# Kernel tuning notes

Measured on AMD Instinct MI355X. Metric: run time of the kernel, lower is better.

Reference implementation:

```python
import jax, jax.numpy as jnp
import numpy as np

HEADS = 20
NUM_AOE = 16
NUM_IP = 16


def setup_inputs() -> dict:
    key = jax.random.key(0)
    ks = jax.random.split(key, 7)
    B, Sq, H = 8, 4096, 1280
    Skv, C = 109, 768
    scale = 0.02
    return {
        "hidden_states": jax.random.normal(ks[0], (B, Sq, H), jnp.float32),
        "encoder_hidden_states": jax.random.normal(ks[1], (B, Skv, C), jnp.float32),
        "Wq": jax.random.normal(ks[2], (H, H), jnp.float32) * scale,
        "Wk": jax.random.normal(ks[3], (C, H), jnp.float32) * scale,
        "Wv": jax.random.normal(ks[4], (C, H), jnp.float32) * scale,
        "Wo": jax.random.normal(ks[5], (H, H), jnp.float32) * scale,
        "bo": jnp.zeros((H,), jnp.float32),
    }


def reference(hidden_states, encoder_hidden_states, Wq, Wk, Wv, Wo, bo):
    B, Sq, H = hidden_states.shape
    Skv = encoder_hidden_states.shape[1]
    head_dim = H // HEADS
    residual = hidden_states

    # projections (no bias on q/k/v, as in diffusers SD attention)
    q = (hidden_states @ Wq).reshape(B, Sq, HEADS, head_dim).transpose(0, 2, 1, 3)
    k = (encoder_hidden_states @ Wk).reshape(B, Skv, HEADS, head_dim).transpose(0, 2, 1, 3)
    v = (encoder_hidden_states @ Wv).reshape(B, Skv, HEADS, head_dim).transpose(0, 2, 1, 3)

    # manual attention: QK^T / sqrt(d), softmax
    scores = jnp.einsum("bhqd,bhkd->bhqk", q, k) / jnp.sqrt(jnp.asarray(head_dim, q.dtype))
    probs = jax.nn.softmax(scores, axis=-1)

    # frequency_mode != 'both': rescale aoe (first NUM_AOE) and image (last NUM_IP)
    # key-token ranges post-softmax, then renormalize. scale_aoe = scale_ip = 1
    # in this config, but the renormalization math is kept faithfully.
    scale_aoe = jnp.asarray(1.0, probs.dtype)
    scale_ip = jnp.asarray(1.0, probs.dtype)
    idx = jnp.arange(Skv)
    scale_vector = jnp.where(idx < NUM_AOE, scale_aoe, 1.0)
    scale_vector = jnp.where(idx >= Skv - NUM_IP, scale_vector * scale_ip, scale_vector)
    probs = probs * scale_vector  # broadcasts over (B, HEADS, Sq, Skv)
    probs = probs / probs.sum(axis=-1, keepdims=True)

    out = jnp.einsum("bhqk,bhkd->bhqd", probs, v)
    out = out.transpose(0, 2, 1, 3).reshape(B, Sq, H)
    out = out @ Wo + bo
    # residual connection, rescale_output_factor = 1.0
    return out + residual
```

## Files before the change

### kernel.cpp

```cpp
#include <hip/hip_runtime.h>
#include <hip/hip_bf16.h>

typedef unsigned short u16;
typedef __attribute__((ext_vector_type(8))) short short8;
typedef __attribute__((ext_vector_type(4))) short short4v;
typedef __attribute__((ext_vector_type(4))) float f32x4;

#define HEADS 20
#define HD 64
#define BB 8
#define SQ 4096
#define HDIM 1280
#define SKV 109
#define CDIM 768
#define SKV_PAD 128
#define SKV_T 112

#define SBAR() asm volatile("s_barrier" ::: "memory")

static __device__ __forceinline__ u16 f2bf(float x) {
  union { __hip_bfloat16 h; u16 u; } cv;
  cv.h = __float2bfloat16(x);
  return cv.u;
}

static __device__ __forceinline__ void gll16(const void* g, void* l) {
  __builtin_amdgcn_global_load_lds(
      (const __attribute__((address_space(1))) unsigned int*)g,
      (__attribute__((address_space(3))) unsigned int*)l, 16, 0, 0);
}

__global__ __launch_bounds__(256) void tcvt(const float* __restrict__ W,
                                            u16* __restrict__ out, int K, int N,
                                            float scale) {
  __shared__ float t[32][33];
  int tx = threadIdx.x & 31, ty = threadIdx.x >> 5;
  int n0 = blockIdx.x * 32, k0 = blockIdx.y * 32;
#pragma unroll
  for (int i = 0; i < 32; i += 8)
    t[ty + i][tx] = W[(size_t)(k0 + ty + i) * N + n0 + tx];
  __syncthreads();
#pragma unroll
  for (int i = 0; i < 32; i += 8)
    out[(size_t)(n0 + ty + i) * K + k0 + tx] = f2bf(t[tx][ty + i] * scale);
}

__global__ __launch_bounds__(256) void ehs_prep(const float* __restrict__ e,
                                                u16* __restrict__ out) {
  int idx = blockIdx.x * 256 + threadIdx.x;
  if (idx >= BB * SKV_PAD * CDIM / 4) return;
  int c4 = idx * 4;
  int b = c4 / (SKV_PAD * CDIM);
  int rem = c4 - b * (SKV_PAD * CDIM);
  int s = rem / CDIM;
  int c = rem - s * CDIM;
  short4v o = {0, 0, 0, 0};
  if (s < SKV) {
    f32x4 v = *(const f32x4*)(e + ((size_t)b * SKV + s) * CDIM + c);
#pragma unroll
    for (int j = 0; j < 4; j++) o[j] = (short)f2bf(v[j]);
  }
  *(short4v*)&out[c4] = o;
}

__global__ __launch_bounds__(256) void hscvt(const float* __restrict__ in,
                                             u16* __restrict__ out) {
  const size_t total = (size_t)BB * SQ * HDIM;
  size_t step = (size_t)gridDim.x * 256 * 8;
  for (size_t i = ((size_t)blockIdx.x * 256 + threadIdx.x) * 8; i < total;
       i += step) {
    f32x4 a = *(const f32x4*)(in + i);
    f32x4 b = *(const f32x4*)(in + i + 4);
    short8 o;
#pragma unroll
    for (int j = 0; j < 4; j++) {
      o[j] = (short)f2bf(a[j]);
      o[j + 4] = (short)f2bf(b[j]);
    }
    *(short8*)&out[i] = o;
  }
}


template <int MODE>
__global__ __launch_bounds__(512, 4)
void gemm_v2(const u16* __restrict__ A, const u16* __restrict__ Bt,
             void* __restrict__ outp, int K, int ntn,
             const float* __restrict__ bias, const float* __restrict__ resid) {
  __shared__ u16 lds[3][12288];
  const int tid = threadIdx.x;
  const int wid = tid >> 6, lane = tid & 63;
  const int wm = wid >> 2, wn = wid & 3;
  const int g = lane >> 4, r = lane & 15;

  const int nwg = gridDim.x;
  const int orig = blockIdx.x;
  const int wg = (orig & 7) * (nwg >> 3) + (orig >> 3);
  const int mt = wg / ntn, nt = wg - mt * ntn;
  const int row0 = mt * 128, col0 = nt * 256;

  const u16* Ag = A + (size_t)row0 * K;
  const u16* Bg = Bt + (size_t)col0 * K;
  const int NT = K >> 5;

  const int cx = (g * 8) ^ (((r >> 1) & 3) << 3);

  const int sa_row = tid >> 2;
  const int sa_sc = (tid & 3) ^ ((tid >> 3) & 3);
  const int sb_row1 = (tid + 512) >> 2;
  const int sb_sc1 = ((tid + 512) & 3) ^ (((tid + 512) >> 3) & 3);

  f32x4 acc[4][4] = {};

  auto stage = [&](int buf, int kt) {
    gll16(Ag + (size_t)sa_row * K + kt + sa_sc * 8, &lds[buf][tid * 8]);
    gll16(Bg + (size_t)sa_row * K + kt + sa_sc * 8, &lds[buf][4096 + tid * 8]);
    gll16(Bg + (size_t)sb_row1 * K + kt + sb_sc1 * 8,
          &lds[buf][4096 + (tid + 512) * 8]);
  };

  stage(0, 0);
  stage(1, 32);
  asm volatile("s_waitcnt vmcnt(3)" ::: "memory");
  SBAR();

  int buf = 0;
  for (int t = 0; t < NT; ++t) {
    int nb = buf + 2;
    if (nb >= 3) nb -= 3;
    if (t + 2 < NT) stage(nb, (t + 2) * 32);

    short8 a[4], b[4];
#pragma unroll
    for (int mi = 0; mi < 4; ++mi)
      a[mi] = *(short8*)&lds[buf][(wm * 64 + mi * 16 + r) * 32 + cx];
#pragma unroll
    for (int nf = 0; nf < 4; ++nf)
      b[nf] = *(short8*)&lds[buf][4096 + (wn * 64 + nf * 16 + r) * 32 + cx];

    __builtin_amdgcn_s_setprio(1);
#pragma unroll
    for (int mi = 0; mi < 4; ++mi)
#pragma unroll
      for (int nf = 0; nf < 4; ++nf)
        acc[mi][nf] = __builtin_amdgcn_mfma_f32_16x16x32_bf16(a[mi], b[nf],
                                                              acc[mi][nf], 0, 0, 0);
    __builtin_amdgcn_s_setprio(0);

    if (t < NT - 2)
      asm volatile("s_waitcnt vmcnt(3)" ::: "memory");
    else
      asm volatile("s_waitcnt vmcnt(0)" ::: "memory");
    SBAR();
    buf = (buf + 1 == 3) ? 0 : buf + 1;
  }

  if constexpr (MODE == 0) {
    u16* O = (u16*)outp;
#pragma unroll
    for (int mi = 0; mi < 4; ++mi)
#pragma unroll
      for (int i = 0; i < 4; ++i) {
        size_t m = row0 + wm * 64 + mi * 16 + g * 4 + i;
        size_t base = m * HDIM + col0 + wn * 64 + r;
#pragma unroll
        for (int nf = 0; nf < 4; ++nf)
          O[base + nf * 16] = f2bf(acc[mi][nf][i]);
      }
  } else {
    float* O = (float*)outp;
#pragma unroll
    for (int mi = 0; mi < 4; ++mi)
#pragma unroll
      for (int i = 0; i < 4; ++i) {
        size_t m = row0 + wm * 64 + mi * 16 + g * 4 + i;
        size_t base = m * HDIM + col0 + wn * 64 + r;
#pragma unroll
        for (int nf = 0; nf < 4; ++nf) {
          int col = col0 + wn * 64 + nf * 16 + r;
          O[base + nf * 16] = acc[mi][nf][i] + bias[col] + resid[base + nf * 16];
        }
      }
  }
}

template <int MODE>
__global__ __launch_bounds__(256, 4)
void gemm_glds(const u16* __restrict__ A, const u16* __restrict__ Bt,
               void* __restrict__ outp, int K, int ntn) {
  __shared__ u16 Alds[128 * 32];
  __shared__ u16 Blds[128 * 32];
  const int tid = threadIdx.x;
  const int wid = tid >> 6, lane = tid & 63;
  const int wm = wid >> 1, wn = wid & 1;
  const int g = lane >> 4, r = lane & 15;

  const int nwg = gridDim.x;
  const int orig = blockIdx.x;
  const int wg = (orig & 7) * (nwg >> 3) + (orig >> 3);
  const int mt = wg / ntn, nt = wg - mt * ntn;
  const int row0 = mt * 128, col0 = nt * 128;
  const int erow = tid >> 2, ecol = (tid & 3) * 8;

  f32x4 acc[4][4] = {};

  for (int kt = 0; kt < K; kt += 32) {
    const u16* ag = A + (size_t)(row0 + erow) * K + kt + ecol;
    const u16* bg = Bt + (size_t)(col0 + erow) * K + kt + ecol;
    gll16(ag, &Alds[erow * 32 + ecol]);
    gll16(ag + (size_t)64 * K, &Alds[(erow + 64) * 32 + ecol]);
    gll16(bg, &Blds[erow * 32 + ecol]);
    gll16(bg + (size_t)64 * K, &Blds[(erow + 64) * 32 + ecol]);
    __syncthreads();

    short8 afr[4], bfr[4];
#pragma unroll
    for (int mi = 0; mi < 4; mi++)
      afr[mi] = *(short8*)&Alds[(wm * 64 + mi * 16 + r) * 32 + g * 8];
#pragma unroll
    for (int ni = 0; ni < 4; ni++)
      bfr[ni] = *(short8*)&Blds[(wn * 64 + ni * 16 + r) * 32 + g * 8];
#pragma unroll
    for (int mi = 0; mi < 4; mi++)
#pragma unroll
      for (int ni = 0; ni < 4; ni++)
        acc[mi][ni] = __builtin_amdgcn_mfma_f32_16x16x32_bf16(afr[mi], bfr[ni],
                                                              acc[mi][ni], 0, 0, 0);
    __syncthreads();
  }

  u16* O = (u16*)outp;
#pragma unroll
  for (int mi = 0; mi < 4; mi++)
#pragma unroll
    for (int i = 0; i < 4; i++) {
      int m = row0 + wm * 64 + mi * 16 + g * 4 + i;
      int b = m >> 7, skv = m & 127;
#pragma unroll
      for (int ni = 0; ni < 4; ni++) {
        int col = col0 + wn * 64 + ni * 16 + r;
        int hh = col >> 6, d = col & 63;
        size_t addr;
        if constexpr (MODE == 1)
          addr = (((size_t)b * HEADS + hh) * SKV_PAD + skv) * HD + d;
        else
          addr = (((size_t)b * HEADS + hh) * HD + d) * SKV_PAD + skv;
        O[addr] = f2bf(acc[mi][ni][i]);
      }
    }
}

__global__ __launch_bounds__(256, 2)
void attn_kernel(const u16* __restrict__ q, const u16* __restrict__ kh,
                 const u16* __restrict__ vt, u16* __restrict__ o) {
  __shared__ u16 Klds[SKV_T * 72];
  __shared__ u16 Vlds[HD * 136];
  __shared__ u16 Plds[4 * 16 * 136];
  const int tid = threadIdx.x;
  const int wid = tid >> 6, lane = tid & 63;
  const int g = lane >> 4, r = lane & 15;
  const int qt = blockIdx.x;
  const int bh = blockIdx.y;
  const int b = bh / HEADS, h = bh - b * HEADS;

  const u16* kg = kh + (size_t)bh * SKV_PAD * HD;
  for (int i = tid; i < SKV_T * 8; i += 256) {
    int row = i >> 3, c = (i & 7) * 8;
    *(short8*)&Klds[row * 72 + c] = *(const short8*)(kg + row * HD + c);
  }
  const u16* vg = vt + (size_t)bh * HD * SKV_PAD;
  for (int i = tid; i < HD * 16; i += 256) {
    int row = i >> 4, c = (i & 15) * 8;
    *(short8*)&Vlds[row * 136 + c] = *(const short8*)(vg + row * SKV_PAD + c);
  }
  __syncthreads();

  const u16* qg = q + ((size_t)b * SQ + qt * 64 + wid * 16 + r) * HDIM + h * HD + g * 8;
  short8 aq0 = *(const short8*)(qg);
  short8 aq1 = *(const short8*)(qg + 32);

  f32x4 s[7];
#pragma unroll
  for (int nf = 0; nf < 7; nf++) {
    f32x4 z = {0.f, 0.f, 0.f, 0.f};
    short8 k0 = *(short8*)&Klds[(nf * 16 + r) * 72 + g * 8];
    short8 k1 = *(short8*)&Klds[(nf * 16 + r) * 72 + 32 + g * 8];
    z = __builtin_amdgcn_mfma_f32_16x16x32_bf16(aq0, k0, z, 0, 0, 0);
    z = __builtin_amdgcn_mfma_f32_16x16x32_bf16(aq1, k1, z, 0, 0, 0);
    s[nf] = z;
  }

  {
    short4v z = {0, 0, 0, 0};
    *(short4v*)&Plds[(wid * 16 + r) * 136 + 112 + g * 4] = z;
  }

#pragma unroll
  for (int i = 0; i < 4; i++) {
    float pv[7];
    float mx = -1e30f;
#pragma unroll
    for (int nf = 0; nf < 7; nf++) {
      float v = s[nf][i];
      if (nf == 6 && r >= 13) v = -1e30f;
      pv[nf] = v;
      mx = fmaxf(mx, v);
    }
#pragma unroll
    for (int d = 1; d < 16; d <<= 1) mx = fmaxf(mx, __shfl_xor(mx, d, 64));
    float sum = 0.f;
#pragma unroll
    for (int nf = 0; nf < 7; nf++) {
      float e = (nf == 6 && r >= 13) ? 0.f : __expf(pv[nf] - mx);
      pv[nf] = e;
      sum += e;
    }
#pragma unroll
    for (int d = 1; d < 16; d <<= 1) sum += __shfl_xor(sum, d, 64);
    float is = 1.f / sum;
#pragma unroll
    for (int nf = 0; nf < 7; nf++)
      Plds[(wid * 16 + g * 4 + i) * 136 + nf * 16 + r] = f2bf(pv[nf] * is);
  }
  __syncthreads();

  f32x4 oacc[4] = {};
#pragma unroll
  for (int kk = 0; kk < 4; kk++) {
    short8 ap = *(short8*)&Plds[(wid * 16 + r) * 136 + kk * 32 + g * 8];
#pragma unroll
    for (int nf = 0; nf < 4; nf++) {
      short8 bv = *(short8*)&Vlds[(nf * 16 + r) * 136 + kk * 32 + g * 8];
      oacc[nf] = __builtin_amdgcn_mfma_f32_16x16x32_bf16(ap, bv, oacc[nf], 0, 0, 0);
    }
  }
  u16* og = o + ((size_t)b * SQ + qt * 64 + wid * 16) * HDIM + h * HD;
#pragma unroll
  for (int nf = 0; nf < 4; nf++)
#pragma unroll
    for (int i = 0; i < 4; i++)
      og[(size_t)(g * 4 + i) * HDIM + nf * 16 + r] = f2bf(oacc[nf][i]);
}

extern "C" void kernel_launch(void* const* d_in, const int* in_sizes, int n_in,
                              void* d_out, int out_size, void* d_ws, size_t ws_size,
                              hipStream_t stream) {
  const float* hs  = (const float*)d_in[0];
  const float* ehs = (const float*)d_in[1];
  const float* Wq  = (const float*)d_in[2];
  const float* Wk  = (const float*)d_in[3];
  const float* Wv  = (const float*)d_in[4];
  const float* Wo  = (const float*)d_in[5];
  const float* bo  = (const float*)d_in[6];

  char* ws = (char*)d_ws;
  size_t off = 0;
  auto alloc = [&](size_t elems) {
    u16* p = (u16*)(ws + off);
    off += ((elems * 2 + 255) / 256) * 256;
    return p;
  };
  u16* wqt  = alloc((size_t)HDIM * HDIM);
  u16* wot  = alloc((size_t)HDIM * HDIM);
  u16* wkt  = alloc((size_t)HDIM * CDIM);
  u16* wvt  = alloc((size_t)HDIM * CDIM);
  u16* ehsp = alloc((size_t)BB * SKV_PAD * CDIM);
  u16* khb  = alloc((size_t)BB * HEADS * SKV_PAD * HD);
  u16* vtb  = alloc((size_t)BB * HEADS * HD * SKV_PAD);
  u16* qb   = alloc((size_t)BB * SQ * HDIM);
  u16* ao   = alloc((size_t)BB * SQ * HDIM);
  u16* hsb  = ao;

  tcvt<<<dim3(HDIM / 32, HDIM / 32), 256, 0, stream>>>(Wq, wqt, HDIM, HDIM, 0.125f);
  tcvt<<<dim3(HDIM / 32, CDIM / 32), 256, 0, stream>>>(Wk, wkt, CDIM, HDIM, 1.0f);
  tcvt<<<dim3(HDIM / 32, CDIM / 32), 256, 0, stream>>>(Wv, wvt, CDIM, HDIM, 1.0f);
  tcvt<<<dim3(HDIM / 32, HDIM / 32), 256, 0, stream>>>(Wo, wot, HDIM, HDIM, 1.0f);
  ehs_prep<<<dim3((BB * SKV_PAD * CDIM / 4 + 255) / 256), 256, 0, stream>>>(ehs, ehsp);
  hscvt<<<dim3(2048), 256, 0, stream>>>(hs, hsb);

  gemm_glds<1><<<dim3(80), 256, 0, stream>>>(ehsp, wkt, khb, CDIM, 10);
  gemm_glds<2><<<dim3(80), 256, 0, stream>>>(ehsp, wvt, vtb, CDIM, 10);
  gemm_v2<0><<<dim3(1280), 512, 0, stream>>>(hsb, wqt, qb, HDIM, 5, nullptr, nullptr);
  attn_kernel<<<dim3(SQ / 64, BB * HEADS), 256, 0, stream>>>(qb, khb, vtb, ao);
  gemm_v2<3><<<dim3(1280), 512, 0, stream>>>(ao, wot, (void*)d_out, HDIM, 5, bo, hs);
}
```

Measured before the change: 442.3 us.

## Fuse fp32-to-bf16 hidden-state conversion into Q projection GEMM loader

Removes the standalone hscvt kernel and has the Q-projection GEMM read fp32 hidden states straight from global memory, converting to bf16 in registers before writing to LDS. The A-tile pipeline becomes register-staged with even/odd buffers, while the B tile keeps using direct global-to-LDS loads. This avoids writing and re-reading the bf16 copy of the large activation tensor, but the GEMM now reads twice the A bytes and adds conversion ALU work and extra waits inside the main loop.

```diff
diff --git a/kernel.cpp b/kernel.cpp
--- a/kernel.cpp
+++ b/kernel.cpp
@@ -63,28 +63,10 @@
   *(short4v*)&out[c4] = o;
 }
 
-__global__ __launch_bounds__(256) void hscvt(const float* __restrict__ in,
-                                             u16* __restrict__ out) {
-  const size_t total = (size_t)BB * SQ * HDIM;
-  size_t step = (size_t)gridDim.x * 256 * 8;
-  for (size_t i = ((size_t)blockIdx.x * 256 + threadIdx.x) * 8; i < total;
-       i += step) {
-    f32x4 a = *(const f32x4*)(in + i);
-    f32x4 b = *(const f32x4*)(in + i + 4);
-    short8 o;
-#pragma unroll
-    for (int j = 0; j < 4; j++) {
-      o[j] = (short)f2bf(a[j]);
-      o[j + 4] = (short)f2bf(b[j]);
-    }
-    *(short8*)&out[i] = o;
-  }
-}
-
-
-template <int MODE>
+
+template <typename AT, int MODE>
 __global__ __launch_bounds__(512, 4)
-void gemm_v2(const u16* __restrict__ A, const u16* __restrict__ Bt,
+void gemm_v2(const AT* __restrict__ A, const u16* __restrict__ Bt,
              void* __restrict__ outp, int K, int ntn,
              const float* __restrict__ bias, const float* __restrict__ resid) {
   __shared__ u16 lds[3][12288];
@@ -99,37 +81,27 @@
   const int mt = wg / ntn, nt = wg - mt * ntn;
   const int row0 = mt * 128, col0 = nt * 256;
 
-  const u16* Ag = A + (size_t)row0 * K;
+  const AT* Ag = A + (size_t)row0 * K;
   const u16* Bg = Bt + (size_t)col0 * K;
   const int NT = K >> 5;
 
   const int cx = (g * 8) ^ (((r >> 1) & 3) << 3);
 
   const int sa_row = tid >> 2;
-  const int sa_sc = (tid & 3) ^ ((tid >> 3) & 3);
+  const int sa_gc = tid & 3;
+  const int sa_wc = sa_gc ^ ((sa_row >> 1) & 3);
   const int sb_row1 = (tid + 512) >> 2;
   const int sb_sc1 = ((tid + 512) & 3) ^ (((tid + 512) >> 3) & 3);
 
   f32x4 acc[4][4] = {};
 
-  auto stage = [&](int buf, int kt) {
-    gll16(Ag + (size_t)sa_row * K + kt + sa_sc * 8, &lds[buf][tid * 8]);
-    gll16(Bg + (size_t)sa_row * K + kt + sa_sc * 8, &lds[buf][4096 + tid * 8]);
+  auto stageB = [&](int b2, int kt) {
+    gll16(Bg + (size_t)sa_row * K + kt + sa_wc * 8, &lds[b2][4096 + tid * 8]);
     gll16(Bg + (size_t)sb_row1 * K + kt + sb_sc1 * 8,
-          &lds[buf][4096 + (tid + 512) * 8]);
+          &lds[b2][4096 + (tid + 512) * 8]);
   };
 
-  stage(0, 0);
-  stage(1, 32);
-  asm volatile("s_waitcnt vmcnt(3)" ::: "memory");
-  SBAR();
-
-  int buf = 0;
-  for (int t = 0; t < NT; ++t) {
-    int nb = buf + 2;
-    if (nb >= 3) nb -= 3;
-    if (t + 2 < NT) stage(nb, (t + 2) * 32);
-
+  auto compute = [&](int buf) {
     short8 a[4], b[4];
 #pragma unroll
     for (int mi = 0; mi < 4; ++mi)
@@ -137,7 +109,6 @@
 #pragma unroll
     for (int nf = 0; nf < 4; ++nf)
       b[nf] = *(short8*)&lds[buf][4096 + (wn * 64 + nf * 16 + r) * 32 + cx];
-
     __builtin_amdgcn_s_setprio(1);
 #pragma unroll
     for (int mi = 0; mi < 4; ++mi)
@@ -146,13 +117,101 @@
         acc[mi][nf] = __builtin_amdgcn_mfma_f32_16x16x32_bf16(a[mi], b[nf],
                                                               acc[mi][nf], 0, 0, 0);
     __builtin_amdgcn_s_setprio(0);
-
-    if (t < NT - 2)
-      asm volatile("s_waitcnt vmcnt(3)" ::: "memory");
-    else
-      asm volatile("s_waitcnt vmcnt(0)" ::: "memory");
+  };
+
+  if constexpr (sizeof(AT) == 2) {
+    auto stage = [&](int buf, int kt) {
+      gll16((const u16*)Ag + (size_t)sa_row * K + kt + sa_wc * 8,
+            &lds[buf][tid * 8]);
+      stageB(buf, kt);
+    };
+    stage(0, 0);
+    stage(1, 32);
+    asm volatile("s_waitcnt vmcnt(3)" ::: "memory");
     SBAR();
-    buf = (buf + 1 == 3) ? 0 : buf + 1;
+    int buf = 0;
+    for (int t = 0; t < NT; ++t) {
+      int nb = buf + 2;
+      if (nb >= 3) nb -= 3;
+      if (t + 2 < NT) stage(nb, (t + 2) * 32);
+      compute(buf);
+      if (t < NT - 2)
+        asm volatile("s_waitcnt vmcnt(3)" ::: "memory");
+      else
+        asm volatile("s_waitcnt vmcnt(0)" ::: "memory");
+      SBAR();
+      buf = (buf + 1 == 3) ? 0 : buf + 1;
+    }
+  } else {
+    f32x4 vaE0, vaE1, vaO0, vaO1;
+    auto issueA = [&](f32x4& v0, f32x4& v1, int kt) {
+      const float* p = (const float*)Ag + (size_t)sa_row * K + kt + sa_gc * 8;
+      v0 = *(const f32x4*)p;
+      v1 = *(const f32x4*)(p + 4);
+    };
+    auto writeA = [&](int b1, const f32x4& v0, const f32x4& v1) {
+      short8 o;
+#pragma unroll
+      for (int j = 0; j < 4; ++j) {
+        o[j] = (short)f2bf(v0[j]);
+        o[j + 4] = (short)f2bf(v1[j]);
+      }
+      *(short8*)&lds[b1][(sa_row * 4 + sa_wc) * 8] = o;
+    };
+
+    issueA(vaE0, vaE1, 0);
+    stageB(0, 0);
+    issueA(vaO0, vaO1, 32);
+    stageB(1, 32);
+    asm volatile("s_waitcnt vmcnt(4)" ::: "memory");
+    writeA(0, vaE0, vaE1);
+    asm volatile("s_waitcnt lgkmcnt(0)" ::: "memory");
+    SBAR();
+
+    int buf = 0;
+    for (int t = 0; t < NT; t += 2) {
+      {
+        int b2 = buf + 2;
+        if (b2 >= 3) b2 -= 3;
+        if (t + 2 < NT) {
+          issueA(vaE0, vaE1, (t + 2) * 32);
+          stageB(b2, (t + 2) * 32);
+        }
+        compute(buf);
+        if (t + 2 < NT)
+          asm volatile("s_waitcnt vmcnt(4)" ::: "memory");
+        else
+          asm volatile("s_waitcnt vmcnt(0)" ::: "memory");
+        int b1 = buf + 1;
+        if (b1 >= 3) b1 -= 3;
+        writeA(b1, vaO0, vaO1);
+        asm volatile("s_waitcnt lgkmcnt(0)" ::: "memory");
+        SBAR();
+        buf = (buf + 1 == 3) ? 0 : buf + 1;
+      }
+      {
+        int t1 = t + 1;
+        int b2 = buf + 2;
+        if (b2 >= 3) b2 -= 3;
+        if (t1 + 2 < NT) {
+          issueA(vaO0, vaO1, (t1 + 2) * 32);
+          stageB(b2, (t1 + 2) * 32);
+        }
+        compute(buf);
+        if (t1 + 2 < NT)
+          asm volatile("s_waitcnt vmcnt(4)" ::: "memory");
+        else
+          asm volatile("s_waitcnt vmcnt(0)" ::: "memory");
+        if (t1 + 1 < NT) {
+          int b1 = buf + 1;
+          if (b1 >= 3) b1 -= 3;
+          writeA(b1, vaE0, vaE1);
+        }
+        asm volatile("s_waitcnt lgkmcnt(0)" ::: "memory");
+        SBAR();
+        buf = (buf + 1 == 3) ? 0 : buf + 1;
+      }
+    }
   }
 
   if constexpr (MODE == 0) {
@@ -369,18 +428,18 @@
   u16* vtb  = alloc((size_t)BB * HEADS * HD * SKV_PAD);
   u16* qb   = alloc((size_t)BB * SQ * HDIM);
   u16* ao   = alloc((size_t)BB * SQ * HDIM);
-  u16* hsb  = ao;
 
   tcvt<<<dim3(HDIM / 32, HDIM / 32), 256, 0, stream>>>(Wq, wqt, HDIM, HDIM, 0.125f);
   tcvt<<<dim3(HDIM / 32, CDIM / 32), 256, 0, stream>>>(Wk, wkt, CDIM, HDIM, 1.0f);
   tcvt<<<dim3(HDIM / 32, CDIM / 32), 256, 0, stream>>>(Wv, wvt, CDIM, HDIM, 1.0f);
   tcvt<<<dim3(HDIM / 32, HDIM / 32), 256, 0, stream>>>(Wo, wot, HDIM, HDIM, 1.0f);
   ehs_prep<<<dim3((BB * SKV_PAD * CDIM / 4 + 255) / 256), 256, 0, stream>>>(ehs, ehsp);
-  hscvt<<<dim3(2048), 256, 0, stream>>>(hs, hsb);
 
   gemm_glds<1><<<dim3(80), 256, 0, stream>>>(ehsp, wkt, khb, CDIM, 10);
   gemm_glds<2><<<dim3(80), 256, 0, stream>>>(ehsp, wvt, vtb, CDIM, 10);
-  gemm_v2<0><<<dim3(1280), 512, 0, stream>>>(hsb, wqt, qb, HDIM, 5, nullptr, nullptr);
+  gemm_v2<float, 0><<<dim3(1280), 512, 0, stream>>>(hs, wqt, qb, HDIM, 5,
+                                                    nullptr, nullptr);
   attn_kernel<<<dim3(SQ / 64, BB * HEADS), 256, 0, stream>>>(qb, khb, vtb, ao);
-  gemm_v2<3><<<dim3(1280), 512, 0, stream>>>(ao, wot, (void*)d_out, HDIM, 5, bo, hs);
-}
+  gemm_v2<u16, 3><<<dim3(1280), 512, 0, stream>>>(ao, wot, (void*)d_out, HDIM, 5,
+                                                  bo, hs);
+}
```

Measured after the change: 496.1 us. +12.2%, slower.

## Merge K/V projection launches and loop attention over query tiles

Applied to the files above, without the earlier changes.

The separate K and V projection GEMM launches are merged into one 160-block launch that picks K or V by block index. The attention kernel now gives each block 8 query tiles instead of 1, so the K/V LDS staging is loaded once and reused across tiles, with the next Q fragment prefetched. Output is staged through LDS so it can be written as 16-byte row chunks instead of scattered 2-byte stores. The grid shrinks from 64x160 to 8x160 blocks, which lowers parallelism. The per-iteration Plds and Olds reuse relies on each wave only touching its own rows, since there is no barrier inside the loop.

```diff
diff --git a/kernel.cpp b/kernel.cpp
--- a/kernel.cpp
+++ b/kernel.cpp
@@ -184,10 +184,10 @@
   }
 }
 
-template <int MODE>
 __global__ __launch_bounds__(256, 4)
-void gemm_glds(const u16* __restrict__ A, const u16* __restrict__ Bt,
-               void* __restrict__ outp, int K, int ntn) {
+void gemm_kv(const u16* __restrict__ A, const u16* __restrict__ Kt,
+             const u16* __restrict__ Vt, u16* __restrict__ khb,
+             u16* __restrict__ vtb) {
   __shared__ u16 Alds[128 * 32];
   __shared__ u16 Blds[128 * 32];
   const int tid = threadIdx.x;
@@ -195,12 +195,14 @@
   const int wm = wid >> 1, wn = wid & 1;
   const int g = lane >> 4, r = lane & 15;
 
-  const int nwg = gridDim.x;
-  const int orig = blockIdx.x;
-  const int wg = (orig & 7) * (nwg >> 3) + (orig >> 3);
-  const int mt = wg / ntn, nt = wg - mt * ntn;
+  const int half = blockIdx.x >= 80 ? 1 : 0;
+  const u16* Bt = half ? Vt : Kt;
+  const int orig = blockIdx.x - half * 80;
+  const int wg = (orig & 7) * 10 + (orig >> 3);
+  const int mt = wg / 10, nt = wg - mt * 10;
   const int row0 = mt * 128, col0 = nt * 128;
   const int erow = tid >> 2, ecol = (tid & 3) * 8;
+  const int K = CDIM;
 
   f32x4 acc[4][4] = {};
 
@@ -229,7 +231,7 @@
     __syncthreads();
   }
 
-  u16* O = (u16*)outp;
+  u16* O = half ? vtb : khb;
 #pragma unroll
   for (int mi = 0; mi < 4; mi++)
 #pragma unroll
@@ -241,10 +243,10 @@
         int col = col0 + wn * 64 + ni * 16 + r;
         int hh = col >> 6, d = col & 63;
         size_t addr;
-        if constexpr (MODE == 1)
+        if (half)
+          addr = (((size_t)b * HEADS + hh) * HD + d) * SKV_PAD + skv;
+        else
           addr = (((size_t)b * HEADS + hh) * SKV_PAD + skv) * HD + d;
-        else
-          addr = (((size_t)b * HEADS + hh) * HD + d) * SKV_PAD + skv;
         O[addr] = f2bf(acc[mi][ni][i]);
       }
     }
@@ -256,12 +258,13 @@
   __shared__ u16 Klds[SKV_T * 72];
   __shared__ u16 Vlds[HD * 136];
   __shared__ u16 Plds[4 * 16 * 136];
+  __shared__ u16 Olds[4 * 16 * 72];
   const int tid = threadIdx.x;
   const int wid = tid >> 6, lane = tid & 63;
   const int g = lane >> 4, r = lane & 15;
-  const int qt = blockIdx.x;
   const int bh = blockIdx.y;
   const int b = bh / HEADS, h = bh - b * HEADS;
+  const int qt0 = blockIdx.x * 8;
 
   const u16* kg = kh + (size_t)bh * SKV_PAD * HD;
   for (int i = tid; i < SKV_T * 8; i += 256) {
@@ -273,73 +276,89 @@
     int row = i >> 4, c = (i & 15) * 8;
     *(short8*)&Vlds[row * 136 + c] = *(const short8*)(vg + row * SKV_PAD + c);
   }
-  __syncthreads();
-
-  const u16* qg = q + ((size_t)b * SQ + qt * 64 + wid * 16 + r) * HDIM + h * HD + g * 8;
-  short8 aq0 = *(const short8*)(qg);
-  short8 aq1 = *(const short8*)(qg + 32);
-
-  f32x4 s[7];
-#pragma unroll
-  for (int nf = 0; nf < 7; nf++) {
-    f32x4 z = {0.f, 0.f, 0.f, 0.f};
-    short8 k0 = *(short8*)&Klds[(nf * 16 + r) * 72 + g * 8];
-    short8 k1 = *(short8*)&Klds[(nf * 16 + r) * 72 + 32 + g * 8];
-    z = __builtin_amdgcn_mfma_f32_16x16x32_bf16(aq0, k0, z, 0, 0, 0);
-    z = __builtin_amdgcn_mfma_f32_16x16x32_bf16(aq1, k1, z, 0, 0, 0);
-    s[nf] = z;
-  }
-
   {
     short4v z = {0, 0, 0, 0};
     *(short4v*)&Plds[(wid * 16 + r) * 136 + 112 + g * 4] = z;
   }
-
-#pragma unroll
-  for (int i = 0; i < 4; i++) {
-    float pv[7];
-    float mx = -1e30f;
+  __syncthreads();
+
+  const u16* qbase = q + ((size_t)b * SQ + wid * 16 + r) * HDIM + h * HD + g * 8;
+  short8 aq0 = *(const short8*)(qbase + (size_t)qt0 * 64 * HDIM);
+  short8 aq1 = *(const short8*)(qbase + (size_t)qt0 * 64 * HDIM + 32);
+
+#pragma unroll 1
+  for (int qs = 0; qs < 8; ++qs) {
+    const int qt = qt0 + qs;
+
+    f32x4 s[7];
 #pragma unroll
     for (int nf = 0; nf < 7; nf++) {
-      float v = s[nf][i];
-      if (nf == 6 && r >= 13) v = -1e30f;
-      pv[nf] = v;
-      mx = fmaxf(mx, v);
-    }
-#pragma unroll
-    for (int d = 1; d < 16; d <<= 1) mx = fmaxf(mx, __shfl_xor(mx, d, 64));
-    float sum = 0.f;
-#pragma unroll
-    for (int nf = 0; nf < 7; nf++) {
-      float e = (nf == 6 && r >= 13) ? 0.f : __expf(pv[nf] - mx);
-      pv[nf] = e;
-      sum += e;
-    }
-#pragma unroll
-    for (int d = 1; d < 16; d <<= 1) sum += __shfl_xor(sum, d, 64);
-    float is = 1.f / sum;
-#pragma unroll
-    for (int nf = 0; nf < 7; nf++)
-      Plds[(wid * 16 + g * 4 + i) * 136 + nf * 16 + r] = f2bf(pv[nf] * is);
-  }
-  __syncthreads();
-
-  f32x4 oacc[4] = {};
-#pragma unroll
-  for (int kk = 0; kk < 4; kk++) {
-    short8 ap = *(short8*)&Plds[(wid * 16 + r) * 136 + kk * 32 + g * 8];
-#pragma unroll
-    for (int nf = 0; nf < 4; nf++) {
-      short8 bv = *(short8*)&Vlds[(nf * 16 + r) * 136 + kk * 32 + g * 8];
-      oacc[nf] = __builtin_amdgcn_mfma_f32_16x16x32_bf16(ap, bv, oacc[nf], 0, 0, 0);
-    }
-  }
-  u16* og = o + ((size_t)b * SQ + qt * 64 + wid * 16) * HDIM + h * HD;
-#pragma unroll
-  for (int nf = 0; nf < 4; nf++)
-#pragma unroll
-    for (int i = 0; i < 4; i++)
-      og[(size_t)(g * 4 + i) * HDIM + nf * 16 + r] = f2bf(oacc[nf][i]);
+      f32x4 z = {0.f, 0.f, 0.f, 0.f};
+      short8 k0 = *(short8*)&Klds[(nf * 16 + r) * 72 + g * 8];
+      short8 k1 = *(short8*)&Klds[(nf * 16 + r) * 72 + 32 + g * 8];
+      z = __builtin_amdgcn_mfma_f32_16x16x32_bf16(aq0, k0, z, 0, 0, 0);
+      z = __builtin_amdgcn_mfma_f32_16x16x32_bf16(aq1, k1, z, 0, 0, 0);
+      s[nf] = z;
+    }
+
+    if (qs + 1 < 8) {
+      aq0 = *(const short8*)(qbase + (size_t)(qt + 1) * 64 * HDIM);
+      aq1 = *(const short8*)(qbase + (size_t)(qt + 1) * 64 * HDIM + 32);
+    }
+
+#pragma unroll
+    for (int i = 0; i < 4; i++) {
+      float pv[7];
+      float mx = -1e30f;
+#pragma unroll
+      for (int nf = 0; nf < 7; nf++) {
+        float v = s[nf][i];
+        if (nf == 6 && r >= 13) v = -1e30f;
+        pv[nf] = v;
+        mx = fmaxf(mx, v);
+      }
+#pragma unroll
+      for (int d = 1; d < 16; d <<= 1) mx = fmaxf(mx, __shfl_xor(mx, d, 64));
+      float sum = 0.f;
+#pragma unroll
+      for (int nf = 0; nf < 7; nf++) {
+        float e = (nf == 6 && r >= 13) ? 0.f : __expf(pv[nf] - mx);
+        pv[nf] = e;
+        sum += e;
+      }
+#pragma unroll
+      for (int d = 1; d < 16; d <<= 1) sum += __shfl_xor(sum, d, 64);
+      float is = 1.f / sum;
+#pragma unroll
+      for (int nf = 0; nf < 7; nf++)
+        Plds[(wid * 16 + g * 4 + i) * 136 + nf * 16 + r] = f2bf(pv[nf] * is);
+    }
+
+    f32x4 oacc[4] = {};
+#pragma unroll
+    for (int kk = 0; kk < 4; kk++) {
+      short8 ap = *(short8*)&Plds[(wid * 16 + r) * 136 + kk * 32 + g * 8];
+#pragma unroll
+      for (int nf = 0; nf < 4; nf++) {
+        short8 bv = *(short8*)&Vlds[(nf * 16 + r) * 136 + kk * 32 + g * 8];
+        oacc[nf] = __builtin_amdgcn_mfma_f32_16x16x32_bf16(ap, bv, oacc[nf], 0, 0, 0);
+      }
+    }
+
+    u16* st = &Olds[wid * 16 * 72];
+#pragma unroll
+    for (int nf = 0; nf < 4; nf++)
+#pragma unroll
+      for (int i = 0; i < 4; i++)
+        st[(g * 4 + i) * 72 + nf * 16 + r] = f2bf(oacc[nf][i]);
+    u16* og = o + ((size_t)b * SQ + qt * 64 + wid * 16) * HDIM + h * HD;
+#pragma unroll
+    for (int j = 0; j < 2; ++j) {
+      int chunk = lane + j * 64;
+      int row = chunk >> 3, cc = (chunk & 7) * 8;
+      *(short8*)&og[(size_t)row * HDIM + cc] = *(short8*)&st[row * 72 + cc];
+    }
+  }
 }
 
 extern "C" void kernel_launch(void* const* d_in, const int* in_sizes, int n_in,
@@ -378,9 +397,8 @@
   ehs_prep<<<dim3((BB * SKV_PAD * CDIM / 4 + 255) / 256), 256, 0, stream>>>(ehs, ehsp);
   hscvt<<<dim3(2048), 256, 0, stream>>>(hs, hsb);
 
-  gemm_glds<1><<<dim3(80), 256, 0, stream>>>(ehsp, wkt, khb, CDIM, 10);
-  gemm_glds<2><<<dim3(80), 256, 0, stream>>>(ehsp, wvt, vtb, CDIM, 10);
+  gemm_kv<<<dim3(160), 256, 0, stream>>>(ehsp, wkt, wvt, khb, vtb);
   gemm_v2<0><<<dim3(1280), 512, 0, stream>>>(hsb, wqt, qb, HDIM, 5, nullptr, nullptr);
-  attn_kernel<<<dim3(SQ / 64, BB * HEADS), 256, 0, stream>>>(qb, khb, vtb, ao);
+  attn_kernel<<<dim3(SQ / 512, BB * HEADS), 256, 0, stream>>>(qb, khb, vtb, ao);
   gemm_v2<3><<<dim3(1280), 512, 0, stream>>>(ao, wot, (void*)d_out, HDIM, 5, bo, hs);
 }
```

New measurement: 426.7 us. -3.5%, faster.
